# Kernel tuning notes

Measured on AMD Instinct MI355X. Metric: run time of the kernel, lower is better.

Reference implementation:

```python
import math
import jax, jax.numpy as jnp
import numpy as np

B, N, DIM_IN, DIM_OUT = 16, 2048, 512, 512
D_K, N_HEADS = 10, 2
D_HEAD = D_K // N_HEADS  # 5


def setup_inputs() -> dict:
    key = jax.random.key(0)
    ks = jax.random.split(key, 11)
    s_in = 1.0 / math.sqrt(DIM_IN)
    s_dk = 1.0 / math.sqrt(D_K)
    s_20 = 1.0 / math.sqrt(20)
    return {
        "x": jax.random.normal(ks[0], (B, N, DIM_IN), jnp.float32),
        "Wq": jax.random.normal(ks[1], (DIM_IN, D_K), jnp.float32) * s_in,
        "bq": jax.random.normal(ks[2], (D_K,), jnp.float32) * s_in,
        "Wk": jax.random.normal(ks[3], (DIM_IN, D_K), jnp.float32) * s_in,
        "bk": jax.random.normal(ks[4], (D_K,), jnp.float32) * s_in,
        "Wv": jax.random.normal(ks[5], (DIM_IN, D_K), jnp.float32) * s_in,
        "bv": jax.random.normal(ks[6], (D_K,), jnp.float32) * s_in,
        "Wm1": jax.random.normal(ks[7], (D_K, 20), jnp.float32) * s_dk,
        "bm1": jax.random.normal(ks[8], (20,), jnp.float32) * s_dk,
        "Wm2": jax.random.normal(ks[9], (20, DIM_OUT), jnp.float32) * s_20,
        "bm2": jax.random.normal(ks[10], (DIM_OUT,), jnp.float32) * s_20,
    }


def reference(x, Wq, bq, Wk, bk, Wv, bv, Wm1, bm1, Wm2, bm2):
    b, n, _ = x.shape
    # project and split heads: [B, n, d_k] -> [B, h, n, d_head]
    def heads(w, bias):
        return (x @ w + bias).reshape(b, n, N_HEADS, D_HEAD).transpose(0, 2, 1, 3)
    q, k, v = heads(Wq, bq), heads(Wk, bk), heads(Wv, bv)
    # sin-activated scores, then causal mask + softmax
    scores = jnp.sin(jnp.einsum("bhqd,bhkd->bhqk", q, k) / math.sqrt(D_HEAD))
    causal = jnp.tril(jnp.ones((n, n), bool))  # nopeak mask, k=0
    scores = jnp.where(causal, scores, jnp.float32(-1e9))
    attn = jax.nn.softmax(scores, axis=-1)
    vals = jnp.einsum("bhqk,bhkd->bhqd", attn, v)
    concat = vals.transpose(0, 2, 1, 3).reshape(b, n, D_K)
    # MLP head: leaky_relu (slope 0.01) then linear
    h1 = jax.nn.leaky_relu(concat @ Wm1 + bm1, negative_slope=0.01)
    return h1 @ Wm2 + bm2
```

## Files before the change

### kernel.cpp

```cpp
#include <hip/hip_runtime.h>
#include <math.h>

#define BB   16
#define NN   2048
#define DIN  512
#define DKK  10
#define NHD  2
#define DH   5
#define HID  20
#define DOUT 512
#define BH   32
#define KC   256
#define NKC  8
#define CK   128
#define XSTR 132

#define QKV_ELEMS  ((size_t)3*BH*NN*8)
#define PART_ELEMS ((size_t)NKC*BH*NN*8)

__global__ __launch_bounds__(256) void pack_w_kernel(
    const float* __restrict__ Wq, const float* __restrict__ Wk,
    const float* __restrict__ Wv, float* __restrict__ Wpack)
{
    const int idx = blockIdx.x*256 + threadIdx.x;
    const int j = idx >> 5, c = idx & 31;
    float v = 0.f;
    if (c < 10)      v = Wq[j*DKK + c];
    else if (c < 20) v = Wk[j*DKK + (c-10)];
    else if (c < 30) v = Wv[j*DKK + (c-20)];
    Wpack[idx] = v;
}

__global__ __launch_bounds__(256) void proj_kernel(
    const float* __restrict__ x, const float* __restrict__ Wpack,
    const float* __restrict__ bq, const float* __restrict__ bk,
    const float* __restrict__ bv, float* __restrict__ qkv)
{
    __shared__ float xs[32*XSTR];
    __shared__ float ws[CK*32];
    const int t  = threadIdx.x;
    const int tl = t & 31;
    const int r  = t >> 5;
    const int tok0 = blockIdx.x * 32;

    float4 acc = make_float4(0.f, 0.f, 0.f, 0.f);

    for (int ch = 0; ch < DIN/CK; ++ch){
        __syncthreads();
        #pragma unroll
        for (int i=0;i<4;i++){
            const int f = t + i*256;
            const int xtok = f >> 5, c4 = f & 31;
            const float4 v = *(const float4*)(x + (size_t)(tok0+xtok)*DIN + ch*CK + c4*4);
            *(float4*)(xs + xtok*XSTR + c4*4) = v;
        }
        #pragma unroll
        for (int i=0;i<4;i++){
            const int f = t + i*256;
            const int row = f >> 3, c4 = f & 7;
            const float4 v = *(const float4*)(Wpack + (size_t)(ch*CK+row)*32 + c4*4);
            *(float4*)(ws + row*32 + c4*4) = v;
        }
        __syncthreads();

        #pragma unroll 8
        for (int kk = 0; kk < CK; kk += 4){
            const float4 xv = *(const float4*)(xs + tl*XSTR + kk);
            const float4 w0 = *(const float4*)(ws + (kk+0)*32 + r*4);
            const float4 w1 = *(const float4*)(ws + (kk+1)*32 + r*4);
            const float4 w2 = *(const float4*)(ws + (kk+2)*32 + r*4);
            const float4 w3 = *(const float4*)(ws + (kk+3)*32 + r*4);
            acc.x = fmaf(xv.x, w0.x, acc.x);
            acc.y = fmaf(xv.x, w0.y, acc.y);
            acc.z = fmaf(xv.x, w0.z, acc.z);
            acc.w = fmaf(xv.x, w0.w, acc.w);
            acc.x = fmaf(xv.y, w1.x, acc.x);
            acc.y = fmaf(xv.y, w1.y, acc.y);
            acc.z = fmaf(xv.y, w1.z, acc.z);
            acc.w = fmaf(xv.y, w1.w, acc.w);
            acc.x = fmaf(xv.z, w2.x, acc.x);
            acc.y = fmaf(xv.z, w2.y, acc.y);
            acc.z = fmaf(xv.z, w2.z, acc.z);
            acc.w = fmaf(xv.z, w2.w, acc.w);
            acc.x = fmaf(xv.w, w3.x, acc.x);
            acc.y = fmaf(xv.w, w3.y, acc.y);
            acc.z = fmaf(xv.w, w3.z, acc.z);
            acc.w = fmaf(xv.w, w3.w, acc.w);
        }
    }

    const float qs = 0.44721359549995793f;
    const int tok = tok0 + tl;
    const int b   = tok >> 11;
    const int n   = tok & (NN-1);
    const float av[4] = {acc.x, acc.y, acc.z, acc.w};
    #pragma unroll
    for (int i=0;i<4;i++){
        const int c = r*4 + i;
        if (c >= 30) continue;
        const int mat = c / 10;
        const int d10 = c - mat*10;
        const int h   = d10 / 5;
        const int dd  = d10 - h*5;
        float v = av[i] + ((mat==0) ? bq[d10] : (mat==1) ? bk[d10] : bv[d10]);
        if (mat==0) v *= qs;
        qkv[(size_t)mat*BH*NN*8 + (((size_t)(b*NHD+h))*NN + n)*8 + dd] = v;
    }
}

__global__ __launch_bounds__(64) void attn_kernel(
    const float* __restrict__ qkv, float* __restrict__ part)
{
    const int qt   = blockIdx.x;
    const int kc   = blockIdx.y;
    const int bh   = blockIdx.z;
    const int lane = threadIdx.x;
    const int qtile0 = qt*64;
    const int k0     = kc*KC;
    if (k0 > qtile0 + 63) return;

    const int q = qtile0 + lane;
    const float* qr = qkv + ((size_t)bh*NN + q)*8;
    const float4 qv = *(const float4*)qr;
    const float  q4 = qr[4];

    const float* kbase = qkv + (size_t)BH*NN*8 + (size_t)bh*NN*8;
    const float* vbase = kbase + (size_t)BH*NN*8;
    const int kend = (k0+KC < qtile0+64) ? (k0+KC) : (qtile0+64);

    float denom=0.f, a0=0.f, a1=0.f, a2=0.f, a3=0.f, a4=0.f;
    #pragma unroll 4
    for (int k=k0; k<kend; ++k){
        const float* kr = kbase + (size_t)k*8;
        const float* vr = vbase + (size_t)k*8;
        float s = qv.x*kr[0] + qv.y*kr[1] + qv.z*kr[2] + qv.w*kr[3] + q4*kr[4];
        float e = __expf(__sinf(s));
        e = (k <= q) ? e : 0.f;
        denom += e;
        a0 = fmaf(e, vr[0], a0);
        a1 = fmaf(e, vr[1], a1);
        a2 = fmaf(e, vr[2], a2);
        a3 = fmaf(e, vr[3], a3);
        a4 = fmaf(e, vr[4], a4);
    }
    float* pr = part + (((size_t)kc*BH + bh)*NN + q)*8;
    *(float4*)pr = make_float4(a0,a1,a2,a3);
    pr[4] = a4;
    pr[5] = denom;
}

__global__ __launch_bounds__(256) void h1_kernel(
    const float* __restrict__ part,
    const float* __restrict__ Wm1, const float* __restrict__ bm1,
    float* __restrict__ h1buf)
{
    const int tok = blockIdx.x*256 + threadIdx.x;
    const int b   = tok >> 11;
    const int n   = tok & (NN-1);
    const int nc  = (n >> 8) + 1;

    float vals[DKK];
    #pragma unroll
    for (int h=0;h<NHD;h++){
        const int bh = b*NHD + h;
        float s0=0,s1=0,s2=0,s3=0,s4=0,sd=0;
        for (int c=0;c<nc;c++){
            const float* pr = part + (((size_t)c*BH + bh)*NN + n)*8;
            const float4 p0 = *(const float4*)pr;
            const float4 p1 = *(const float4*)(pr+4);
            s0+=p0.x; s1+=p0.y; s2+=p0.z; s3+=p0.w; s4+=p1.x; sd+=p1.y;
        }
        const float inv = 1.0f / sd;
        vals[h*DH+0]=s0*inv; vals[h*DH+1]=s1*inv; vals[h*DH+2]=s2*inv;
        vals[h*DH+3]=s3*inv; vals[h*DH+4]=s4*inv;
    }

    float h1[HID];
    #pragma unroll
    for (int jo=0;jo<HID;jo++){
        float t = bm1[jo];
        #pragma unroll
        for (int d=0;d<DKK;d++) t = fmaf(vals[d], Wm1[d*HID+jo], t);
        h1[jo] = (t > 0.f) ? t : 0.01f*t;
    }
    float* hr = h1buf + (size_t)tok*HID;
    #pragma unroll
    for (int j5=0;j5<5;j5++)
        *(float4*)(hr + j5*4) = make_float4(h1[j5*4+0],h1[j5*4+1],h1[j5*4+2],h1[j5*4+3]);
}

__global__ __launch_bounds__(256) void out_kernel(
    const float* __restrict__ h1buf,
    const float* __restrict__ Wm2, const float* __restrict__ bm2,
    float* __restrict__ out)
{
    const int wave = threadIdx.x >> 6;
    const int lane = threadIdx.x & 63;
    const int unit = blockIdx.x*4 + wave;
    const int hc   = unit & 1;
    const int tg   = unit >> 1;
    const int o0   = hc*256 + lane*4;

    float4 w2[HID];
    #pragma unroll
    for (int j=0;j<HID;j++) w2[j] = *(const float4*)(Wm2 + j*DOUT + o0);
    const float4 b2 = *(const float4*)(bm2 + o0);

    for (int ti=0; ti<8; ++ti){
        const int tok = tg*8 + ti;
        const float* hr = h1buf + (size_t)tok*HID;
        float4 acc = b2;
        #pragma unroll
        for (int j5=0;j5<5;j5++){
            const float4 hv = *(const float4*)(hr + j5*4);
            const float h0=hv.x, h1v=hv.y, h2=hv.z, h3=hv.w;
            acc.x = fmaf(h0, w2[j5*4+0].x, acc.x);
            acc.y = fmaf(h0, w2[j5*4+0].y, acc.y);
            acc.z = fmaf(h0, w2[j5*4+0].z, acc.z);
            acc.w = fmaf(h0, w2[j5*4+0].w, acc.w);
            acc.x = fmaf(h1v, w2[j5*4+1].x, acc.x);
            acc.y = fmaf(h1v, w2[j5*4+1].y, acc.y);
            acc.z = fmaf(h1v, w2[j5*4+1].z, acc.z);
            acc.w = fmaf(h1v, w2[j5*4+1].w, acc.w);
            acc.x = fmaf(h2, w2[j5*4+2].x, acc.x);
            acc.y = fmaf(h2, w2[j5*4+2].y, acc.y);
            acc.z = fmaf(h2, w2[j5*4+2].z, acc.z);
            acc.w = fmaf(h2, w2[j5*4+2].w, acc.w);
            acc.x = fmaf(h3, w2[j5*4+3].x, acc.x);
            acc.y = fmaf(h3, w2[j5*4+3].y, acc.y);
            acc.z = fmaf(h3, w2[j5*4+3].z, acc.z);
            acc.w = fmaf(h3, w2[j5*4+3].w, acc.w);
        }
        *(float4*)(out + (size_t)tok*DOUT + o0) = acc;
    }
}

extern "C" void kernel_launch(void* const* d_in, const int* in_sizes, int n_in,
                              void* d_out, int out_size, void* d_ws, size_t ws_size,
                              hipStream_t stream) {
    const float* x   = (const float*)d_in[0];
    const float* Wq  = (const float*)d_in[1];
    const float* bq  = (const float*)d_in[2];
    const float* Wk  = (const float*)d_in[3];
    const float* bk  = (const float*)d_in[4];
    const float* Wv  = (const float*)d_in[5];
    const float* bv  = (const float*)d_in[6];
    const float* Wm1 = (const float*)d_in[7];
    const float* bm1 = (const float*)d_in[8];
    const float* Wm2 = (const float*)d_in[9];
    const float* bm2 = (const float*)d_in[10];
    float* out = (float*)d_out;

    float* qkv   = (float*)d_ws;
    float* part  = qkv + QKV_ELEMS;
    float* Wpack = part + PART_ELEMS;
    float* h1buf = qkv;

    pack_w_kernel<<<dim3(64), dim3(256), 0, stream>>>(Wq, Wk, Wv, Wpack);
    proj_kernel<<<dim3(1024), dim3(256), 0, stream>>>(x, Wpack, bq, bk, bv, qkv);
    attn_kernel<<<dim3(32, NKC, BH), dim3(64), 0, stream>>>(qkv, part);
    h1_kernel<<<dim3(128), dim3(256), 0, stream>>>(part, Wm1, bm1, h1buf);
    out_kernel<<<dim3(2048), dim3(256), 0, stream>>>(h1buf, Wm2, bm2, out);
}
```

Baseline: 292.9 us.

## Restructure projection to per-thread tokens and stage attention K/V in LDS

The projection kernel now assigns one token per thread, with 30 register accumulators and only the packed weights staged in shared memory, launched on 128 blocks. The attention kernel now uses 256-thread blocks that cooperatively load a 256-key chunk of K and V into shared memory, replacing per-lane broadcast global loads. The aim is more register-level reuse in the projection and fewer redundant global reads of K/V in attention. The risks are that each projection thread reads its own strided row of x, so loads are poorly coalesced, and that 128 blocks leave many CUs idle. Larger attention blocks also do more causal-masked work near the diagonal.

```diff
diff --git a/kernel.cpp b/kernel.cpp
--- a/kernel.cpp
+++ b/kernel.cpp
@@ -12,8 +12,7 @@
 #define BH   32
 #define KC   256
 #define NKC  8
-#define CK   128
-#define XSTR 132
+#define PCK  128
 
 #define QKV_ELEMS  ((size_t)3*BH*NN*8)
 #define PART_ELEMS ((size_t)NKC*BH*NN*8)
@@ -36,112 +35,107 @@
     const float* __restrict__ bq, const float* __restrict__ bk,
     const float* __restrict__ bv, float* __restrict__ qkv)
 {
-    __shared__ float xs[32*XSTR];
-    __shared__ float ws[CK*32];
-    const int t  = threadIdx.x;
-    const int tl = t & 31;
-    const int r  = t >> 5;
-    const int tok0 = blockIdx.x * 32;
-
-    float4 acc = make_float4(0.f, 0.f, 0.f, 0.f);
-
-    for (int ch = 0; ch < DIN/CK; ++ch){
+    __shared__ float ws[PCK*32];
+    const int t   = threadIdx.x;
+    const int tok = blockIdx.x*256 + t;
+    const float* xr = x + (size_t)tok*DIN;
+
+    float acc[30];
+    #pragma unroll
+    for (int o=0;o<30;o++) acc[o]=0.f;
+
+    for (int ch=0; ch<DIN/PCK; ++ch){
         __syncthreads();
-        #pragma unroll
-        for (int i=0;i<4;i++){
-            const int f = t + i*256;
-            const int xtok = f >> 5, c4 = f & 31;
-            const float4 v = *(const float4*)(x + (size_t)(tok0+xtok)*DIN + ch*CK + c4*4);
-            *(float4*)(xs + xtok*XSTR + c4*4) = v;
+        const float4* wsrc = (const float4*)(Wpack + (size_t)ch*PCK*32);
+        #pragma unroll
+        for (int i=0;i<4;i++) ((float4*)ws)[t + i*256] = wsrc[t + i*256];
+        __syncthreads();
+
+        const float* xc = xr + ch*PCK;
+        float4 xa0=*(const float4*)(xc+ 0), xa1=*(const float4*)(xc+ 4),
+               xa2=*(const float4*)(xc+ 8), xa3=*(const float4*)(xc+12);
+        #pragma unroll
+        for (int g=0; g<PCK/16; ++g){
+            float4 xb0,xb1,xb2,xb3;
+            if (g < PCK/16-1){
+                const float* p = xc + (g+1)*16;
+                xb0=*(const float4*)(p+ 0); xb1=*(const float4*)(p+ 4);
+                xb2=*(const float4*)(p+ 8); xb3=*(const float4*)(p+12);
+            }
+            const float xs16[16] = {xa0.x,xa0.y,xa0.z,xa0.w, xa1.x,xa1.y,xa1.z,xa1.w,
+                                    xa2.x,xa2.y,xa2.z,xa2.w, xa3.x,xa3.y,xa3.z,xa3.w};
+            #pragma unroll
+            for (int j=0;j<16;j++){
+                const float xj = xs16[j];
+                const float* wrow = ws + (g*16+j)*32;
+                #pragma unroll
+                for (int o=0;o<30;o++) acc[o] = fmaf(xj, wrow[o], acc[o]);
+            }
+            if (g < PCK/16-1){ xa0=xb0; xa1=xb1; xa2=xb2; xa3=xb3; }
         }
-        #pragma unroll
-        for (int i=0;i<4;i++){
-            const int f = t + i*256;
-            const int row = f >> 3, c4 = f & 7;
-            const float4 v = *(const float4*)(Wpack + (size_t)(ch*CK+row)*32 + c4*4);
-            *(float4*)(ws + row*32 + c4*4) = v;
-        }
-        __syncthreads();
-
-        #pragma unroll 8
-        for (int kk = 0; kk < CK; kk += 4){
-            const float4 xv = *(const float4*)(xs + tl*XSTR + kk);
-            const float4 w0 = *(const float4*)(ws + (kk+0)*32 + r*4);
-            const float4 w1 = *(const float4*)(ws + (kk+1)*32 + r*4);
-            const float4 w2 = *(const float4*)(ws + (kk+2)*32 + r*4);
-            const float4 w3 = *(const float4*)(ws + (kk+3)*32 + r*4);
-            acc.x = fmaf(xv.x, w0.x, acc.x);
-            acc.y = fmaf(xv.x, w0.y, acc.y);
-            acc.z = fmaf(xv.x, w0.z, acc.z);
-            acc.w = fmaf(xv.x, w0.w, acc.w);
-            acc.x = fmaf(xv.y, w1.x, acc.x);
-            acc.y = fmaf(xv.y, w1.y, acc.y);
-            acc.z = fmaf(xv.y, w1.z, acc.z);
-            acc.w = fmaf(xv.y, w1.w, acc.w);
-            acc.x = fmaf(xv.z, w2.x, acc.x);
-            acc.y = fmaf(xv.z, w2.y, acc.y);
-            acc.z = fmaf(xv.z, w2.z, acc.z);
-            acc.w = fmaf(xv.z, w2.w, acc.w);
-            acc.x = fmaf(xv.w, w3.x, acc.x);
-            acc.y = fmaf(xv.w, w3.y, acc.y);
-            acc.z = fmaf(xv.w, w3.z, acc.z);
-            acc.w = fmaf(xv.w, w3.w, acc.w);
-        }
     }
 
     const float qs = 0.44721359549995793f;
-    const int tok = tok0 + tl;
-    const int b   = tok >> 11;
-    const int n   = tok & (NN-1);
-    const float av[4] = {acc.x, acc.y, acc.z, acc.w};
-    #pragma unroll
-    for (int i=0;i<4;i++){
-        const int c = r*4 + i;
-        if (c >= 30) continue;
+    const int b = tok >> 11;
+    const int n = tok & (NN-1);
+    #pragma unroll
+    for (int c=0;c<30;c++){
         const int mat = c / 10;
         const int d10 = c - mat*10;
         const int h   = d10 / 5;
         const int dd  = d10 - h*5;
-        float v = av[i] + ((mat==0) ? bq[d10] : (mat==1) ? bk[d10] : bv[d10]);
+        float v = acc[c] + ((mat==0) ? bq[d10] : (mat==1) ? bk[d10] : bv[d10]);
         if (mat==0) v *= qs;
         qkv[(size_t)mat*BH*NN*8 + (((size_t)(b*NHD+h))*NN + n)*8 + dd] = v;
     }
 }
 
-__global__ __launch_bounds__(64) void attn_kernel(
+__global__ __launch_bounds__(256) void attn_kernel(
     const float* __restrict__ qkv, float* __restrict__ part)
 {
-    const int qt   = blockIdx.x;
-    const int kc   = blockIdx.y;
-    const int bh   = blockIdx.z;
-    const int lane = threadIdx.x;
-    const int qtile0 = qt*64;
-    const int k0     = kc*KC;
-    if (k0 > qtile0 + 63) return;
-
-    const int q = qtile0 + lane;
+    __shared__ float Ks[KC*8];
+    __shared__ float Vs[KC*8];
+    const int qt = blockIdx.x;
+    const int kc = blockIdx.y;
+    const int bh = blockIdx.z;
+    const int k0 = kc*KC;
+    const int qblk0 = qt*256;
+    if (k0 > qblk0 + 255) return;
+
+    const int t    = threadIdx.x;
+    const int lane = t & 63;
+    const int w    = t >> 6;
+
+    const float* kbase = qkv + (size_t)BH*NN*8 + ((size_t)bh*NN + k0)*8;
+    const float* vbase = kbase + (size_t)BH*NN*8;
+    ((float4*)Ks)[t]     = ((const float4*)kbase)[t];
+    ((float4*)Ks)[t+256] = ((const float4*)kbase)[t+256];
+    ((float4*)Vs)[t]     = ((const float4*)vbase)[t];
+    ((float4*)Vs)[t+256] = ((const float4*)vbase)[t+256];
+    __syncthreads();
+
+    const int q = qblk0 + w*64 + lane;
     const float* qr = qkv + ((size_t)bh*NN + q)*8;
     const float4 qv = *(const float4*)qr;
     const float  q4 = qr[4];
-
-    const float* kbase = qkv + (size_t)BH*NN*8 + (size_t)bh*NN*8;
-    const float* vbase = kbase + (size_t)BH*NN*8;
-    const int kend = (k0+KC < qtile0+64) ? (k0+KC) : (qtile0+64);
+    const int kend = min(KC, qblk0 + (w+1)*64 - k0);
 
     float denom=0.f, a0=0.f, a1=0.f, a2=0.f, a3=0.f, a4=0.f;
     #pragma unroll 4
-    for (int k=k0; k<kend; ++k){
-        const float* kr = kbase + (size_t)k*8;
-        const float* vr = vbase + (size_t)k*8;
-        float s = qv.x*kr[0] + qv.y*kr[1] + qv.z*kr[2] + qv.w*kr[3] + q4*kr[4];
+    for (int kk=0; kk<kend; ++kk){
+        const float4 kv = *(const float4*)(Ks + kk*8);
+        const float  k4 = Ks[kk*8+4];
+        const float4 vv = *(const float4*)(Vs + kk*8);
+        const float  v4 = Vs[kk*8+4];
+        float s = qv.x*kv.x + qv.y*kv.y + qv.z*kv.z + qv.w*kv.w + q4*k4;
         float e = __expf(__sinf(s));
-        e = (k <= q) ? e : 0.f;
+        e = (k0+kk <= q) ? e : 0.f;
         denom += e;
-        a0 = fmaf(e, vr[0], a0);
-        a1 = fmaf(e, vr[1], a1);
-        a2 = fmaf(e, vr[2], a2);
-        a3 = fmaf(e, vr[3], a3);
-        a4 = fmaf(e, vr[4], a4);
+        a0 = fmaf(e, vv.x, a0);
+        a1 = fmaf(e, vv.y, a1);
+        a2 = fmaf(e, vv.z, a2);
+        a3 = fmaf(e, vv.w, a3);
+        a4 = fmaf(e, v4,   a4);
     }
     float* pr = part + (((size_t)kc*BH + bh)*NN + q)*8;
     *(float4*)pr = make_float4(a0,a1,a2,a3);
@@ -257,8 +251,8 @@
     float* h1buf = qkv;
 
     pack_w_kernel<<<dim3(64), dim3(256), 0, stream>>>(Wq, Wk, Wv, Wpack);
-    proj_kernel<<<dim3(1024), dim3(256), 0, stream>>>(x, Wpack, bq, bk, bv, qkv);
-    attn_kernel<<<dim3(32, NKC, BH), dim3(64), 0, stream>>>(qkv, part);
+    proj_kernel<<<dim3(128), dim3(256), 0, stream>>>(x, Wpack, bq, bk, bv, qkv);
+    attn_kernel<<<dim3(NN/256, NKC, BH), dim3(256), 0, stream>>>(qkv, part);
     h1_kernel<<<dim3(128), dim3(256), 0, stream>>>(part, Wm1, bm1, h1buf);
     out_kernel<<<dim3(2048), dim3(256), 0, stream>>>(h1buf, Wm2, bm2, out);
 }
```

Result: slower. 385.6 us (+31.6%).
